# Performance work log

Measured on AMD Instinct MI355X. Metric: run time of the kernel, lower is better.

The kernel has to match this reference:

```python
import jax, jax.numpy as jnp
import numpy as np

N_ATOMS = 50000
N_PAIRS = 1600000
N_BASIS = 128
N_FILTERS = 128
N_RBF = 20
LOG2 = float(np.log(2.0))


def ssp(x):
    # ShiftedSoftplus: softplus(x) - log(2)
    return jax.nn.softplus(x) - LOG2


def setup_inputs() -> dict:
    key = jax.random.key(0)
    ks = jax.random.split(key, 16)

    def lin(k, fan_in, fan_out):
        bound = 1.0 / np.sqrt(fan_in)
        kw, kb = jax.random.split(k)
        W = jax.random.uniform(kw, (fan_in, fan_out), jnp.float32, -bound, bound)
        b = jax.random.uniform(kb, (fan_out,), jnp.float32, -bound, bound)
        return W, b

    W_in, b_in = lin(ks[0], N_BASIS, N_FILTERS)
    Wf1, bf1 = lin(ks[1], N_RBF, N_FILTERS)
    Wf2, bf2 = lin(ks[2], N_FILTERS, N_FILTERS)
    Wo1, bo1 = lin(ks[3], N_FILTERS, N_BASIS)
    Wo2, bo2 = lin(ks[4], N_BASIS, N_BASIS)

    return {
        "x": jax.random.normal(ks[5], (N_ATOMS, N_BASIS), jnp.float32),
        "f_ij": jax.random.uniform(ks[6], (N_PAIRS, N_RBF), jnp.float32),
        "rcut_ij": jax.random.uniform(ks[7], (N_PAIRS,), jnp.float32),
        "W_in": W_in, "b_in": b_in,
        "Wf1": Wf1, "bf1": bf1, "Wf2": Wf2, "bf2": bf2,
        "Wo1": Wo1, "bo1": bo1, "Wo2": Wo2, "bo2": bo2,
        "idx_i": jax.random.randint(ks[8], (N_PAIRS,), 0, N_ATOMS, jnp.int32),
        "idx_j": jax.random.randint(ks[9], (N_PAIRS,), 0, N_ATOMS, jnp.int32),
    }


def reference(x, f_ij, rcut_ij, W_in, b_in, Wf1, bf1, Wf2, bf2, Wo1, bo1, Wo2, bo2, idx_i, idx_j):
    # input_to_feature
    h = x @ W_in + b_in                                  # [N, F]
    # filter network: Linear -> ssp -> Linear, then cutoff scaling
    Wij = ssp(f_ij @ Wf1 + bf1) @ Wf2 + bf2              # [E, F]
    Wij = Wij * rcut_ij[:, None]
    # gather - multiply - scatter_add
    x_ij = h[idx_j] * Wij                                # [E, F]
    agg = jax.ops.segment_sum(x_ij, idx_i, num_segments=h.shape[0])  # [N, F]
    # feature_to_output: Linear -> ssp -> Linear
    out = ssp(agg @ Wo1 + bo1) @ Wo2 + bo2               # [N, B]
    return out
```

## Files before the change

### kernel.cpp

```cpp
#include <hip/hip_runtime.h>
#include <math.h>

#define N_ATOMS 50000
#define N_PAIRS 1600000
#define NF 128
#define NRBF 20
#define NTILES (N_PAIRS / 64)

typedef _Float16 half8 __attribute__((ext_vector_type(8)));
typedef float floatx4 __attribute__((ext_vector_type(4)));

__device__ __forceinline__ float sspf(float x) {
    float t = __expf(-fabsf(x));
    return fmaxf(x, 0.0f) + __logf(1.0f + t) - 0.69314718055994530942f;
}

__device__ __forceinline__ int swz16(int row, int k8) {
    return row * 256 + ((k8 ^ (row & 15)) << 4);
}

template<int NTHR>
__device__ __forceinline__ void stage_w(const float* __restrict__ W, char* dst, int t) {
    for (int i = t; i < 128 * 128; i += NTHR) {
        int c = i & 127, k = i >> 7;
        *(_Float16*)(dst + swz16(c, k >> 3) + ((k & 7) << 1)) = (_Float16)W[k * 128 + c];
    }
}

template<typename TIN, typename TOUT, bool SSP_OUT, bool ZERO>
__global__ __launch_bounds__(256) void gemm_mfma_kernel(
    const TIN* __restrict__ A, const float* __restrict__ W,
    const float* __restrict__ bias, TOUT* __restrict__ out, int M,
    float* __restrict__ zbuf, int zcount4)
{
    __shared__ char sW[32768];
    const int t = threadIdx.x;
    const int w = t >> 6, lane = t & 63, m = lane & 15, q = lane >> 4;

    if (ZERO) {
        float4 z = {0.f, 0.f, 0.f, 0.f};
        for (int i = blockIdx.x * 256 + t; i < zcount4; i += gridDim.x * 256)
            ((float4*)zbuf)[i] = z;
    }
    stage_w<256>(W, sW, t);
    float bv[8];
    #pragma unroll
    for (int g = 0; g < 8; ++g) bv[g] = bias[g * 16 + m];
    __syncthreads();

    const floatx4 zero4 = {0.f, 0.f, 0.f, 0.f};
    const int ntiles = (M + 63) >> 6;
    for (int tile = blockIdx.x; tile < ntiles; tile += gridDim.x) {
        const int arow = tile * 64 + w * 16 + m;
        half8 a[4];
        if (arow < M) {
            const TIN* ap = A + (size_t)arow * 128;
            #pragma unroll
            for (int s = 0; s < 4; ++s) {
                if (sizeof(TIN) == 2) {
                    a[s] = *(const half8*)(ap + s * 32 + q * 8);
                } else {
                    float4 u0 = *(const float4*)((const float*)ap + s * 32 + q * 8);
                    float4 u1 = *(const float4*)((const float*)ap + s * 32 + q * 8 + 4);
                    a[s][0] = (_Float16)u0.x; a[s][1] = (_Float16)u0.y;
                    a[s][2] = (_Float16)u0.z; a[s][3] = (_Float16)u0.w;
                    a[s][4] = (_Float16)u1.x; a[s][5] = (_Float16)u1.y;
                    a[s][6] = (_Float16)u1.z; a[s][7] = (_Float16)u1.w;
                }
            }
        } else {
            #pragma unroll
            for (int s = 0; s < 4; ++s) a[s] = (half8){};
        }
        floatx4 acc[8];
        #pragma unroll
        for (int g = 0; g < 8; ++g) {
            floatx4 c = zero4;
            #pragma unroll
            for (int s = 0; s < 4; ++s) {
                half8 b = *(const half8*)(sW + swz16(g * 16 + m, 4 * s + q));
                c = __builtin_amdgcn_mfma_f32_16x16x32_f16(a[s], b, c, 0, 0, 0);
            }
            acc[g] = c;
        }
        #pragma unroll
        for (int r = 0; r < 4; ++r) {
            const int grow = tile * 64 + w * 16 + q * 4 + r;
            if (grow < M) {
                TOUT* op = out + (size_t)grow * 128;
                #pragma unroll
                for (int g = 0; g < 8; ++g) {
                    float v = acc[g][r] + bv[g];
                    if (SSP_OUT) v = sspf(v);
                    op[g * 16 + m] = (TOUT)v;
                }
            }
        }
    }
}

__global__ __launch_bounds__(256) void edge_kernel(
    const float* __restrict__ f_ij, const float* __restrict__ rcut,
    const float* __restrict__ Wf1, const float* __restrict__ bf1,
    const float* __restrict__ Wf2, const float* __restrict__ bf2,
    const int* __restrict__ idx_i, const int* __restrict__ idx_j,
    const _Float16* __restrict__ h, float* __restrict__ agg)
{
    __shared__ char sW2[32768];
    __shared__ char sS[4][4096];
    const int t = threadIdx.x;
    const int w = t >> 6, lane = t & 63, m = lane & 15, q = lane >> 4;

    stage_w<256>(Wf2, sW2, t);
    half8 bW1[8];
    #pragma unroll
    for (int g = 0; g < 8; ++g) {
        #pragma unroll
        for (int j = 0; j < 8; ++j) {
            int k = q * 8 + j;
            bW1[g][j] = (k < NRBF) ? (_Float16)Wf1[k * 128 + g * 16 + m] : (_Float16)0.0f;
        }
    }
    float bf1r[8], bf2r[8];
    #pragma unroll
    for (int g = 0; g < 8; ++g) { bf1r[g] = bf1[g * 16 + m]; bf2r[g] = bf2[g * 16 + m]; }
    __syncthreads();

    char* mySS = sS[w];
    const floatx4 zero4 = {0.f, 0.f, 0.f, 0.f};
    const float4 fz = {0.f, 0.f, 0.f, 0.f};
    const int stride = gridDim.x;

    float4 f0 = fz, f1 = fz; int4 jj4;
    {
        int e0 = blockIdx.x * 64 + w * 16;
        const float* fb = f_ij + (size_t)(e0 + m) * NRBF + q * 8;
        if (q < 2)      { f0 = *(const float4*)fb; f1 = *(const float4*)(fb + 4); }
        else if (q == 2){ f0 = *(const float4*)fb; }
        jj4 = *(const int4*)&idx_j[e0 + q * 4];
    }

    for (int tile = blockIdx.x; tile < NTILES; tile += stride) {
        const int e0 = tile * 64 + w * 16;
        int ntile = tile + stride; if (ntile >= NTILES) ntile = tile;

        int jj[4] = {jj4.x, jj4.y, jj4.z, jj4.w};
        _Float16 hv[4][8];
        #pragma unroll
        for (int r = 0; r < 4; ++r) {
            const _Float16* hp = h + (size_t)jj[r] * 128;
            #pragma unroll
            for (int g = 0; g < 8; ++g) hv[r][g] = hp[g * 16 + m];
        }
        int4 ii4 = *(const int4*)&idx_i[e0 + q * 4];
        float4 rc4 = *(const float4*)&rcut[e0 + q * 4];

        half8 a1;
        a1[0]=(_Float16)f0.x; a1[1]=(_Float16)f0.y; a1[2]=(_Float16)f0.z; a1[3]=(_Float16)f0.w;
        a1[4]=(_Float16)f1.x; a1[5]=(_Float16)f1.y; a1[6]=(_Float16)f1.z; a1[7]=(_Float16)f1.w;
        floatx4 c1[8];
        #pragma unroll
        for (int g = 0; g < 8; ++g)
            c1[g] = __builtin_amdgcn_mfma_f32_16x16x32_f16(a1, bW1[g], zero4, 0, 0, 0);

        float4 nf0 = fz, nf1 = fz; int4 njj4;
        {
            int ne0 = ntile * 64 + w * 16;
            const float* fb = f_ij + (size_t)(ne0 + m) * NRBF + q * 8;
            if (q < 2)      { nf0 = *(const float4*)fb; nf1 = *(const float4*)(fb + 4); }
            else if (q == 2){ nf0 = *(const float4*)fb; }
            njj4 = *(const int4*)&idx_j[ne0 + q * 4];
        }

        #pragma unroll
        for (int g = 0; g < 8; ++g) {
            #pragma unroll
            for (int r = 0; r < 4; ++r) {
                float v = sspf(c1[g][r] + bf1r[g]);
                *(_Float16*)(mySS + swz16(q * 4 + r, 2 * g + (m >> 3)) + ((m & 7) << 1)) =
                    (_Float16)v;
            }
        }

        half8 a2[4];
        #pragma unroll
        for (int s = 0; s < 4; ++s)
            a2[s] = *(const half8*)(mySS + swz16(m, 4 * s + q));

        floatx4 acc[8];
        #pragma unroll
        for (int g = 0; g < 8; ++g) {
            floatx4 c = zero4;
            #pragma unroll
            for (int s = 0; s < 4; ++s) {
                half8 b = *(const half8*)(sW2 + swz16(g * 16 + m, 4 * s + q));
                c = __builtin_amdgcn_mfma_f32_16x16x32_f16(a2[s], b, c, 0, 0, 0);
            }
            acc[g] = c;
        }

        int ii[4] = {ii4.x, ii4.y, ii4.z, ii4.w};
        float rc[4] = {rc4.x, rc4.y, rc4.z, rc4.w};
        #pragma unroll
        for (int r = 0; r < 4; ++r) {
            float* arow = agg + (size_t)ii[r] * 128;
            #pragma unroll
            for (int g = 0; g < 8; ++g) {
                float wij = (acc[g][r] + bf2r[g]) * rc[r];
                atomicAdd(&arow[g * 16 + m], (float)hv[r][g] * wij);
            }
        }

        f0 = nf0; f1 = nf1; jj4 = njj4;
    }
}

extern "C" void kernel_launch(void* const* d_in, const int* in_sizes, int n_in,
                              void* d_out, int out_size, void* d_ws, size_t ws_size,
                              hipStream_t stream) {
    const float* x     = (const float*)d_in[0];
    const float* f_ij  = (const float*)d_in[1];
    const float* rcutp = (const float*)d_in[2];
    const float* W_in  = (const float*)d_in[3];
    const float* b_in  = (const float*)d_in[4];
    const float* Wf1   = (const float*)d_in[5];
    const float* bf1   = (const float*)d_in[6];
    const float* Wf2   = (const float*)d_in[7];
    const float* bf2   = (const float*)d_in[8];
    const float* Wo1   = (const float*)d_in[9];
    const float* bo1   = (const float*)d_in[10];
    const float* Wo2   = (const float*)d_in[11];
    const float* bo2   = (const float*)d_in[12];
    const int* idx_i   = (const int*)d_in[13];
    const int* idx_j   = (const int*)d_in[14];
    float* out = (float*)d_out;

    float*     agg = (float*)d_ws;
    _Float16*  h   = (_Float16*)((char*)d_ws + (size_t)N_ATOMS * NF * 4);
    _Float16*  tmp = h;

    const int zc4 = N_ATOMS * NF / 4;
    gemm_mfma_kernel<float, _Float16, false, true>
        <<<dim3(782), 256, 0, stream>>>(x, W_in, b_in, h, N_ATOMS, agg, zc4);
    edge_kernel<<<dim3(768), 256, 0, stream>>>(f_ij, rcutp, Wf1, bf1, Wf2, bf2,
                                               idx_i, idx_j, h, agg);
    gemm_mfma_kernel<float, _Float16, true, false>
        <<<dim3(782), 256, 0, stream>>>(agg, Wo1, bo1, tmp, N_ATOMS, nullptr, 0);
    gemm_mfma_kernel<_Float16, float, false, false>
        <<<dim3(782), 256, 0, stream>>>(tmp, Wo2, bo2, out, N_ATOMS, nullptr, 0);
}
```

Measured before the change: 916.2 us.

## Deepen edge-kernel prefetch pipeline and shrink grids for persistent blocks

The edge kernel now prefetches the next tile's h gather rows, idx_i and rcut one iteration ahead, and idx_j two iterations ahead, so the random h gathers overlap with the current tile's MFMA work and atomics. It also gains a launch bound of 2 blocks per SM, and the grid sizes shrink (GEMMs 782→192, edge 768→512) so blocks become grid-stride loops. Weight staging now converts pairs of K rows into half2 stores. The extra prefetched registers (nhv) raise register pressure, and the smaller grids may cut parallelism for the GEMMs.

```diff
diff --git a/kernel.cpp b/kernel.cpp
--- a/kernel.cpp
+++ b/kernel.cpp
@@ -8,6 +8,7 @@
 #define NTILES (N_PAIRS / 64)
 
 typedef _Float16 half8 __attribute__((ext_vector_type(8)));
+typedef _Float16 half2t __attribute__((ext_vector_type(2)));
 typedef float floatx4 __attribute__((ext_vector_type(4)));
 
 __device__ __forceinline__ float sspf(float x) {
@@ -21,9 +22,13 @@
 
 template<int NTHR>
 __device__ __forceinline__ void stage_w(const float* __restrict__ W, char* dst, int t) {
-    for (int i = t; i < 128 * 128; i += NTHR) {
-        int c = i & 127, k = i >> 7;
-        *(_Float16*)(dst + swz16(c, k >> 3) + ((k & 7) << 1)) = (_Float16)W[k * 128 + c];
+    for (int i = t; i < 64 * 128; i += NTHR) {
+        int k2 = i >> 7, c = i & 127;
+        int k = k2 * 2;
+        half2t v;
+        v[0] = (_Float16)W[k * 128 + c];
+        v[1] = (_Float16)W[(k + 1) * 128 + c];
+        *(half2t*)(dst + swz16(c, k >> 3) + ((k & 7) << 1)) = v;
     }
 }
 
@@ -99,7 +104,7 @@
     }
 }
 
-__global__ __launch_bounds__(256) void edge_kernel(
+__global__ __launch_bounds__(256, 2) void edge_kernel(
     const float* __restrict__ f_ij, const float* __restrict__ rcut,
     const float* __restrict__ Wf1, const float* __restrict__ bf1,
     const float* __restrict__ Wf2, const float* __restrict__ bf2,
@@ -129,31 +134,39 @@
     char* mySS = sS[w];
     const floatx4 zero4 = {0.f, 0.f, 0.f, 0.f};
     const float4 fz = {0.f, 0.f, 0.f, 0.f};
-    const int stride = gridDim.x;
-
-    float4 f0 = fz, f1 = fz; int4 jj4;
+    const int S = gridDim.x;
+
+    int tl = blockIdx.x;
+    float4 f0 = fz, f1 = fz;
+    int4 ii4, jj4; float4 rc4;
     {
-        int e0 = blockIdx.x * 64 + w * 16;
+        const int e0 = tl * 64 + w * 16;
         const float* fb = f_ij + (size_t)(e0 + m) * NRBF + q * 8;
         if (q < 2)      { f0 = *(const float4*)fb; f1 = *(const float4*)(fb + 4); }
         else if (q == 2){ f0 = *(const float4*)fb; }
+        ii4 = *(const int4*)&idx_i[e0 + q * 4];
+        rc4 = *(const float4*)&rcut[e0 + q * 4];
         jj4 = *(const int4*)&idx_j[e0 + q * 4];
     }
-
-    for (int tile = blockIdx.x; tile < NTILES; tile += stride) {
-        const int e0 = tile * 64 + w * 16;
-        int ntile = tile + stride; if (ntile >= NTILES) ntile = tile;
-
+    _Float16 hv[4][8];
+    {
         int jj[4] = {jj4.x, jj4.y, jj4.z, jj4.w};
-        _Float16 hv[4][8];
         #pragma unroll
         for (int r = 0; r < 4; ++r) {
             const _Float16* hp = h + (size_t)jj[r] * 128;
             #pragma unroll
             for (int g = 0; g < 8; ++g) hv[r][g] = hp[g * 16 + m];
         }
-        int4 ii4 = *(const int4*)&idx_i[e0 + q * 4];
-        float4 rc4 = *(const float4*)&rcut[e0 + q * 4];
+    }
+    int4 jjv;
+    {
+        const int nt = (tl + S < NTILES) ? tl + S : tl;
+        jjv = *(const int4*)&idx_j[nt * 64 + w * 16 + q * 4];
+    }
+
+    for (; tl < NTILES; tl += S) {
+        const int nx  = (tl + S     < NTILES) ? tl + S     : tl;
+        const int nx2 = (tl + 2 * S < NTILES) ? tl + 2 * S : nx;
 
         half8 a1;
         a1[0]=(_Float16)f0.x; a1[1]=(_Float16)f0.y; a1[2]=(_Float16)f0.z; a1[3]=(_Float16)f0.w;
@@ -163,15 +176,6 @@
         for (int g = 0; g < 8; ++g)
             c1[g] = __builtin_amdgcn_mfma_f32_16x16x32_f16(a1, bW1[g], zero4, 0, 0, 0);
 
-        float4 nf0 = fz, nf1 = fz; int4 njj4;
-        {
-            int ne0 = ntile * 64 + w * 16;
-            const float* fb = f_ij + (size_t)(ne0 + m) * NRBF + q * 8;
-            if (q < 2)      { nf0 = *(const float4*)fb; nf1 = *(const float4*)(fb + 4); }
-            else if (q == 2){ nf0 = *(const float4*)fb; }
-            njj4 = *(const int4*)&idx_j[ne0 + q * 4];
-        }
-
         #pragma unroll
         for (int g = 0; g < 8; ++g) {
             #pragma unroll
@@ -181,12 +185,10 @@
                     (_Float16)v;
             }
         }
-
         half8 a2[4];
         #pragma unroll
         for (int s = 0; s < 4; ++s)
             a2[s] = *(const half8*)(mySS + swz16(m, 4 * s + q));
-
         floatx4 acc[8];
         #pragma unroll
         for (int g = 0; g < 8; ++g) {
@@ -199,6 +201,27 @@
             acc[g] = c;
         }
 
+        float4 nf0 = fz, nf1 = fz;
+        {
+            const int e0 = nx * 64 + w * 16;
+            const float* fb = f_ij + (size_t)(e0 + m) * NRBF + q * 8;
+            if (q < 2)      { nf0 = *(const float4*)fb; nf1 = *(const float4*)(fb + 4); }
+            else if (q == 2){ nf0 = *(const float4*)fb; }
+        }
+        int4  nii4 = *(const int4*)&idx_i[nx * 64 + w * 16 + q * 4];
+        float4 nrc4 = *(const float4*)&rcut[nx * 64 + w * 16 + q * 4];
+        int4  njj  = *(const int4*)&idx_j[nx2 * 64 + w * 16 + q * 4];
+        _Float16 nhv[4][8];
+        {
+            int jj[4] = {jjv.x, jjv.y, jjv.z, jjv.w};
+            #pragma unroll
+            for (int r = 0; r < 4; ++r) {
+                const _Float16* hp = h + (size_t)jj[r] * 128;
+                #pragma unroll
+                for (int g = 0; g < 8; ++g) nhv[r][g] = hp[g * 16 + m];
+            }
+        }
+
         int ii[4] = {ii4.x, ii4.y, ii4.z, ii4.w};
         float rc[4] = {rc4.x, rc4.y, rc4.z, rc4.w};
         #pragma unroll
@@ -211,7 +234,11 @@
             }
         }
 
-        f0 = nf0; f1 = nf1; jj4 = njj4;
+        f0 = nf0; f1 = nf1; ii4 = nii4; rc4 = nrc4; jjv = njj;
+        #pragma unroll
+        for (int r = 0; r < 4; ++r)
+            #pragma unroll
+            for (int g = 0; g < 8; ++g) hv[r][g] = nhv[r][g];
     }
 }
 
@@ -241,11 +268,11 @@
 
     const int zc4 = N_ATOMS * NF / 4;
     gemm_mfma_kernel<float, _Float16, false, true>
-        <<<dim3(782), 256, 0, stream>>>(x, W_in, b_in, h, N_ATOMS, agg, zc4);
-    edge_kernel<<<dim3(768), 256, 0, stream>>>(f_ij, rcutp, Wf1, bf1, Wf2, bf2,
+        <<<dim3(192), 256, 0, stream>>>(x, W_in, b_in, h, N_ATOMS, agg, zc4);
+    edge_kernel<<<dim3(512), 256, 0, stream>>>(f_ij, rcutp, Wf1, bf1, Wf2, bf2,
                                                idx_i, idx_j, h, agg);
     gemm_mfma_kernel<float, _Float16, true, false>
-        <<<dim3(782), 256, 0, stream>>>(agg, Wo1, bo1, tmp, N_ATOMS, nullptr, 0);
+        <<<dim3(192), 256, 0, stream>>>(agg, Wo1, bo1, tmp, N_ATOMS, nullptr, 0);
     gemm_mfma_kernel<_Float16, float, false, false>
-        <<<dim3(782), 256, 0, stream>>>(tmp, Wo2, bo2, out, N_ATOMS, nullptr, 0);
-}
+        <<<dim3(192), 256, 0, stream>>>(tmp, Wo2, bo2, out, N_ATOMS, nullptr, 0);
+}
```

New measurement: 1.189 ms. 29.8% more time.
